# Kernel optimization log

Hardware: AMD Instinct MI355X
Metric: run time of the kernel (lower is better)

The kernel has to match this reference:

```python
import jax, jax.numpy as jnp
import numpy as np

LOSS_WEIGHT = 1.0

# Zero-padded shifts implementing PyTorch cross-correlation stencils.
# _shift_w(x, +1)[..., j] = x[..., j+1] (zero outside), etc.

def _shift_w(x, s):
    if s == 1:
        return jnp.pad(x[..., 1:], ((0, 0), (0, 0), (0, 1)))
    return jnp.pad(x[..., :-1], ((0, 0), (0, 0), (1, 0)))


def _shift_h(x, s):
    if s == 1:
        return jnp.pad(x[..., 1:, :], ((0, 0), (0, 1), (0, 0)))
    return jnp.pad(x[..., :-1, :], ((0, 0), (1, 0), (0, 0)))


def _curvature_loss(prob):
    # prob: [B, H, W]. Fused stencil chain equivalent to the 7 tiny conv2d calls.
    lap = (_shift_h(prob, 1) + _shift_h(prob, -1)
           + _shift_w(prob, 1) + _shift_w(prob, -1) - 4.0 * prob)
    gx = _shift_w(lap, 1) - _shift_w(lap, -1)          # dx = [-1, 0, 1]
    gy = _shift_h(lap, 1) - _shift_h(lap, -1)          # dy = [-1, 0, 1]^T
    hxx = 2.0 * gx - _shift_w(gx, 1) - _shift_w(gx, -1)  # dxx = [-1, 2, -1]
    hyy = 2.0 * gy - _shift_h(gy, 1) - _shift_h(gy, -1)  # dyy = [-1, 2, -1]^T
    hxy = _shift_w(gx, 1) - _shift_w(gx, -1)
    numerator = hxx * (1.0 + gy) ** 2 - 2.0 * hxy * gx * gy + hyy * (1.0 + gx) ** 2
    denominator = 2.0 * (1.0 + gx ** 2 + gy ** 2) ** 1.5
    curvature = numerator / denominator
    neg_curv = jnp.maximum(-curvature, 0.0)
    s = jnp.sum(neg_curv, axis=(1, 2))                              # [B]
    c = jnp.sum(neg_curv != 0, axis=(1, 2)).astype(prob.dtype)      # [B]
    # per-sample masked mean, skipped when no negative curvature
    per_sample = jnp.where(c > 0, s / jnp.maximum(c, 1.0), 0.0)
    return jnp.sum(per_sample)


def setup_inputs() -> dict:
    key = jax.random.key(0)
    k1, k2 = jax.random.split(key)
    pred = jax.random.normal(k1, (8, 4, 1024, 1024), dtype=jnp.float32)
    target = jax.random.randint(k2, (8, 1024, 1024), 0, 4, dtype=jnp.int64)
    return {"pred": pred, "target": target}


def reference(pred, target):
    # softmax=True path; num_classes == 4 branch of the original forward
    p = jax.nn.softmax(pred, axis=1)
    prob_1 = p[:, 1]
    prob_2 = p[:, 1] + p[:, 2]
    prob_3 = p[:, 3]
    loss = (_curvature_loss(prob_1) + _curvature_loss(prob_2)
            + _curvature_loss(prob_3))
    return loss * LOSS_WEIGHT
```

## Files before the change

kernel.cpp:

```cpp
#include <hip/hip_runtime.h>


namespace {
constexpr int H = 1024, W = 1024, B = 8;
constexpr int VALID = 120;
constexpr int NSTRIPS = 9;
constexpr int RCHUNK = 8;
constexpr int NCHUNKS = H / RCHUNK;
constexpr int WPB = 4;
constexpr int NTHREADS = 64 * WPB;
constexpr size_t HW = (size_t)H * W;
}

__device__ __forceinline__ float dpp_left(float x) {
    return __builtin_bit_cast(float,
        __builtin_amdgcn_update_dpp(0, __builtin_bit_cast(int, x),
                                    0x138 , 0xf, 0xf, false));
}
__device__ __forceinline__ float dpp_right(float x) {
    return __builtin_bit_cast(float,
        __builtin_amdgcn_update_dpp(0, __builtin_bit_cast(int, x),
                                    0x130 , 0xf, 0xf, false));
}

__global__ void zero_ws_kernel(unsigned int* ws) {
    if (threadIdx.x < 48) ws[threadIdx.x] = 0u;
}

__device__ __forceinline__ float2 ld2(const float* p) {
    return *(const float2*)p;
}

template <bool RE>
__device__ __forceinline__ void load_row4(const float* __restrict__ basep, int row,
                                          float2 o[4]) {
    const int rc = RE ? min(max(row, 0), H - 1) : row;
    const float* p = basep + (size_t)rc * W;
    o[0] = ld2(p);
    o[1] = ld2(p + HW);
    o[2] = ld2(p + 2 * HW);
    o[3] = ld2(p + 3 * HW);
}

template <bool CE>
__device__ __forceinline__ void softmax_pair(const float2 x[4], bool ok0, bool ok1,
                                             float2 p[3]) {
    const float e0x = __expf(x[0].x), e1x = __expf(x[1].x);
    const float e2x = __expf(x[2].x), e3x = __expf(x[3].x);
    const float e0y = __expf(x[0].y), e1y = __expf(x[1].y);
    const float e2y = __expf(x[2].y), e3y = __expf(x[3].y);
    const float ix = __builtin_amdgcn_rcpf(e0x + e1x + e2x + e3x);
    const float iy = __builtin_amdgcn_rcpf(e0y + e1y + e2y + e3y);
    if (CE) {
        p[0].x = ok0 ? e1x * ix : 0.f;
        p[0].y = ok1 ? e1y * iy : 0.f;
        p[1].x = ok0 ? (e1x + e2x) * ix : 0.f;
        p[1].y = ok1 ? (e1y + e2y) * iy : 0.f;
        p[2].x = ok0 ? e3x * ix : 0.f;
        p[2].y = ok1 ? e3y * iy : 0.f;
    } else {
        p[0].x = e1x * ix;            p[0].y = e1y * iy;
        p[1].x = (e1x + e2x) * ix;    p[1].y = (e1y + e2y) * iy;
        p[2].x = e3x * ix;            p[2].y = e3y * iy;
    }
}

template <bool CE, bool RE>
__device__ __forceinline__ void sweep(const float* __restrict__ pred,
                                      int b, int strip, int chunk, int lane,
                                      float sacc[3], unsigned int cacc[3]) {
    const int r0 = chunk * RCHUNK;
    const int li0 = 2 * lane;
    const int col0 = strip * VALID - 4 + li0;
    const int col1 = col0 + 1;
    const int colC = CE ? min(max(col0, 0), W - 2) : col0;
    const float* basep = pred + (size_t)b * 4 * HW + colC;

    const bool cOK0 = !CE || ((unsigned)col0 < (unsigned)W);
    const bool cOK1 = !CE || ((unsigned)col1 < (unsigned)W);
    const bool aOK0 = (li0 >= 4) && (li0 <= 123) && cOK0;
    const bool aOK1 = (li0 + 1 >= 4) && (li0 + 1 <= 123) && cOK1;
    const float gxpM0 = (!CE || (col0 + 1 < W)) ? 1.f : 0.f;
    const float gxpM1 = (!CE || (col1 + 1 < W)) ? 1.f : 0.f;
    const float gxmM0 = (!CE || (col0 >= 1)) ? 1.f : 0.f;
    const float gxmM1 = (!CE || (col1 >= 1)) ? 1.f : 0.f;

    float2 P[3][3];
    float2 L[6][3];
    float2 Rr[2][4];

    {
        float2 t[4];
        load_row4<RE>(basep, r0 - 3, t);
        const bool ok = !RE || ((unsigned)(r0 - 3) < (unsigned)H);
        softmax_pair<CE || RE>(t, ok && cOK0, ok && cOK1, P[1]);
        load_row4<RE>(basep, r0 - 2, t);
        const bool ok2 = !RE || ((unsigned)(r0 - 2) < (unsigned)H);
        softmax_pair<CE || RE>(t, ok2 && cOK0, ok2 && cOK1, P[2]);
    }
    load_row4<RE>(basep, r0 - 1, Rr[0]);
    load_row4<RE>(basep, r0, Rr[1]);

    auto acc1 = [&](int f, float gx, float gy, float gxp, float gxm,
                    float gyp, float gym, bool aOK) {
        const float hxx = 2.f * gx - gxp - gxm;
        const float hxy = gxp - gxm;
        const float hyy = 2.f * gy - gyp - gym;
        const float oy = 1.f + gy, ox = 1.f + gx;
        const float numer = hxx * oy * oy - 2.f * hxy * gx * gy + hyy * ox * ox;
        const float xx = 1.f + gx * gx + gy * gy;
        const float rs = __builtin_amdgcn_rsqf(xx);
        const float curv = numer * (0.5f * rs * rs * rs);
        const float negc = aOK ? fmaxf(-curv, 0.f) : 0.f;
        sacc[f] += negc;
        cacc[f] += (negc != 0.f) ? 1u : 0u;
    };

    for (int m = 0; m < 2; ++m) {
#pragma unroll
        for (int u = 0; u < 6; ++u) {
            const int y = r0 - 4 + m * 6 + u;
            const bool pok = !RE || ((unsigned)(y + 3) < (unsigned)H);
            softmax_pair<CE || RE>(Rr[u % 2], pok && cOK0, pok && cOK1, P[u % 3]);
            load_row4<RE>(basep, y + 5, Rr[u % 2]);
            const bool lok = !RE || ((unsigned)(y + 2) < (unsigned)H);
#pragma unroll
            for (int f = 0; f < 3; ++f) {
                const float2 top = P[(u + 1) % 3][f];
                const float2 mid = P[(u + 2) % 3][f];
                const float2 bot = P[u % 3][f];
                const float lft = dpp_left(mid.y);
                const float rgt = dpp_right(mid.x);
                const float lx = top.x + bot.x + lft + mid.y - 4.f * mid.x;
                const float ly = top.y + bot.y + mid.x + rgt - 4.f * mid.y;
                if (CE || RE) {
                    L[u][f].x = (lok && cOK0) ? lx : 0.f;
                    L[u][f].y = (lok && cOK1) ? ly : 0.f;
                } else {
                    L[u][f].x = lx;
                    L[u][f].y = ly;
                }
            }
            if (m > 0 || u >= 4) {
                const float gypM = (!RE || (y + 1 < H)) ? 1.f : 0.f;
                const float gymM = (!RE || (y >= 1)) ? 1.f : 0.f;
#pragma unroll
                for (int f = 0; f < 3; ++f) {
                    const float2 lm2 = L[(u + 2) % 6][f];
                    const float2 lm1 = L[(u + 3) % 6][f];
                    const float2 lc  = L[(u + 4) % 6][f];
                    const float2 lp1 = L[(u + 5) % 6][f];
                    const float2 lp2 = L[u % 6][f];
                    const float A  = dpp_left(lc.y);
                    const float Bm = dpp_left(lc.x);
                    const float Bp = dpp_right(lc.x);
                    const float Cc = dpp_right(lc.y);
                    {
                        const float c = lc.x;
                        const float gx = lc.y - A;
                        const float gy = lp1.x - lm1.x;
                        const float gxp = (Bp - c) * gxpM0;
                        const float gxm = (c - Bm) * gxmM0;
                        const float gyp = (lp2.x - c) * gypM;
                        const float gym = (c - lm2.x) * gymM;
                        acc1(f, gx, gy, gxp, gxm, gyp, gym, aOK0);
                    }
                    {
                        const float c = lc.y;
                        const float gx = Bp - lc.x;
                        const float gy = lp1.y - lm1.y;
                        const float gxp = (Cc - c) * gxpM1;
                        const float gxm = (c - A) * gxmM1;
                        const float gyp = (lp2.y - c) * gypM;
                        const float gym = (c - lm2.y) * gymM;
                        acc1(f, gx, gy, gxp, gxm, gyp, gym, aOK1);
                    }
                }
            }
        }
    }
}

__global__ __launch_bounds__(NTHREADS)
void curvature_sweep(const float* __restrict__ pred,
                     float* __restrict__ s_ws,
                     unsigned int* __restrict__ c_ws) {
    __shared__ float redS[3][WPB];
    __shared__ unsigned int redC[3][WPB];

    const int strip = blockIdx.x;
    const int b = blockIdx.z;
    const int tid = threadIdx.x;
    const int wv = tid >> 6, lane = tid & 63;
    const int chunk = blockIdx.y * WPB + wv;

    const bool ce = (strip == 0) || (strip == NSTRIPS - 1);
    const bool re = (chunk == 0) || (chunk == NCHUNKS - 1);

    float sacc[3] = {0.f, 0.f, 0.f};
    unsigned int cacc[3] = {0u, 0u, 0u};
    if (!ce && !re)      sweep<false, false>(pred, b, strip, chunk, lane, sacc, cacc);
    else if (ce && !re)  sweep<true, false>(pred, b, strip, chunk, lane, sacc, cacc);
    else if (!ce && re)  sweep<false, true>(pred, b, strip, chunk, lane, sacc, cacc);
    else                 sweep<true, true>(pred, b, strip, chunk, lane, sacc, cacc);

#pragma unroll
    for (int f = 0; f < 3; ++f) {
        float v = sacc[f];
        unsigned int c = cacc[f];
        for (int off = 32; off > 0; off >>= 1) {
            v += __shfl_xor(v, off, 64);
            c += __shfl_xor(c, off, 64);
        }
        if (lane == 0) { redS[f][wv] = v; redC[f][wv] = c; }
    }
    __syncthreads();
    if (tid < 3) {
        float v = 0.f;
        unsigned int c = 0;
        for (int w2 = 0; w2 < WPB; ++w2) { v += redS[tid][w2]; c += redC[tid][w2]; }
        atomicAdd(&s_ws[b * 3 + tid], v);
        atomicAdd(&c_ws[b * 3 + tid], c);
    }
}

__global__ void finalize_kernel(const float* __restrict__ s_ws,
                                const unsigned int* __restrict__ c_ws,
                                float* __restrict__ out) {
    const int lane = threadIdx.x;
    float v = 0.f;
    if (lane < 24) {
        const float s = s_ws[lane];
        const unsigned int c = c_ws[lane];
        v = (c > 0) ? s / (float)c : 0.f;
    }
    for (int off = 32; off > 0; off >>= 1) v += __shfl_down(v, off, 64);
    if (lane == 0) out[0] = v;
}

extern "C" void kernel_launch(void* const* d_in, const int* in_sizes, int n_in,
                              void* d_out, int out_size, void* d_ws, size_t ws_size,
                              hipStream_t stream) {
    const float* pred = (const float*)d_in[0];
    float* s_ws = (float*)d_ws;
    unsigned int* c_ws = (unsigned int*)((char*)d_ws + 24 * sizeof(float));
    float* out = (float*)d_out;

    hipLaunchKernelGGL(zero_ws_kernel, dim3(1), dim3(64), 0, stream,
                       (unsigned int*)d_ws);
    dim3 grid(NSTRIPS, NCHUNKS / WPB, B);
    hipLaunchKernelGGL(curvature_sweep, grid, dim3(NTHREADS), 0, stream,
                       pred, s_ws, c_ws);
    hipLaunchKernelGGL(finalize_kernel, dim3(1), dim3(64), 0, stream,
                       s_ws, c_ws, out);
}
```

Measured before the change: 68.43 us.

## Double row chunk height and vectorize stencil math with packed float2 ops

Each wave now sweeps 16 rows instead of 8, with the ring buffers resized to 5 slots and an unrolled 10-step inner loop. This cuts the share of halo rows that are recomputed (softmax and Laplacian) per output row. The per-pixel curvature math is rewritten on 2-wide ext_vector floats so the compiler can emit packed FP32 instructions. A min-blocks-per-SM hint is added to launch bounds. In exchange there are half as many work items, which lowers available parallelism, and register pressure may rise.

```diff
diff --git a/kernel.cpp b/kernel.cpp
--- a/kernel.cpp
+++ b/kernel.cpp
@@ -5,13 +5,19 @@
 constexpr int H = 1024, W = 1024, B = 8;
 constexpr int VALID = 120;
 constexpr int NSTRIPS = 9;
-constexpr int RCHUNK = 8;
+constexpr int RCHUNK = 16;
 constexpr int NCHUNKS = H / RCHUNK;
 constexpr int WPB = 4;
 constexpr int NTHREADS = 64 * WPB;
 constexpr size_t HW = (size_t)H * W;
 }
 
+using v2f = __attribute__((ext_vector_type(2))) float;
+
+__device__ __forceinline__ v2f mk2(float a, float b) {
+    v2f r; r.x = a; r.y = b; return r;
+}
+
 __device__ __forceinline__ float dpp_left(float x) {
     return __builtin_bit_cast(float,
         __builtin_amdgcn_update_dpp(0, __builtin_bit_cast(int, x),
@@ -27,48 +33,42 @@
     if (threadIdx.x < 48) ws[threadIdx.x] = 0u;
 }
 
-__device__ __forceinline__ float2 ld2(const float* p) {
-    return *(const float2*)p;
-}
-
 template <bool RE>
 __device__ __forceinline__ void load_row4(const float* __restrict__ basep, int row,
-                                          float2 o[4]) {
+                                          v2f o[4]) {
     const int rc = RE ? min(max(row, 0), H - 1) : row;
     const float* p = basep + (size_t)rc * W;
-    o[0] = ld2(p);
-    o[1] = ld2(p + HW);
-    o[2] = ld2(p + 2 * HW);
-    o[3] = ld2(p + 3 * HW);
-}
-
-template <bool CE>
-__device__ __forceinline__ void softmax_pair(const float2 x[4], bool ok0, bool ok1,
-                                             float2 p[3]) {
+    o[0] = *(const v2f*)p;
+    o[1] = *(const v2f*)(p + HW);
+    o[2] = *(const v2f*)(p + 2 * HW);
+    o[3] = *(const v2f*)(p + 3 * HW);
+}
+
+template <bool EDGE>
+__device__ __forceinline__ void softmax_pair(const v2f x[4], bool ok0, bool ok1,
+                                             v2f p[3]) {
     const float e0x = __expf(x[0].x), e1x = __expf(x[1].x);
     const float e2x = __expf(x[2].x), e3x = __expf(x[3].x);
     const float e0y = __expf(x[0].y), e1y = __expf(x[1].y);
     const float e2y = __expf(x[2].y), e3y = __expf(x[3].y);
     const float ix = __builtin_amdgcn_rcpf(e0x + e1x + e2x + e3x);
     const float iy = __builtin_amdgcn_rcpf(e0y + e1y + e2y + e3y);
-    if (CE) {
-        p[0].x = ok0 ? e1x * ix : 0.f;
-        p[0].y = ok1 ? e1y * iy : 0.f;
-        p[1].x = ok0 ? (e1x + e2x) * ix : 0.f;
-        p[1].y = ok1 ? (e1y + e2y) * iy : 0.f;
-        p[2].x = ok0 ? e3x * ix : 0.f;
-        p[2].y = ok1 ? e3y * iy : 0.f;
+    if (EDGE) {
+        p[0] = mk2(ok0 ? e1x * ix : 0.f,          ok1 ? e1y * iy : 0.f);
+        p[1] = mk2(ok0 ? (e1x + e2x) * ix : 0.f,  ok1 ? (e1y + e2y) * iy : 0.f);
+        p[2] = mk2(ok0 ? e3x * ix : 0.f,          ok1 ? e3y * iy : 0.f);
     } else {
-        p[0].x = e1x * ix;            p[0].y = e1y * iy;
-        p[1].x = (e1x + e2x) * ix;    p[1].y = (e1y + e2y) * iy;
-        p[2].x = e3x * ix;            p[2].y = e3y * iy;
+        p[0] = mk2(e1x * ix,          e1y * iy);
+        p[1] = mk2((e1x + e2x) * ix,  (e1y + e2y) * iy);
+        p[2] = mk2(e3x * ix,          e3y * iy);
     }
 }
 
 template <bool CE, bool RE>
 __device__ __forceinline__ void sweep(const float* __restrict__ pred,
                                       int b, int strip, int chunk, int lane,
-                                      float sacc[3], unsigned int cacc[3]) {
+                                      v2f sacc[3], unsigned int cacc0[3],
+                                      unsigned int cacc1[3]) {
     const int r0 = chunk * RCHUNK;
     const int li0 = 2 * lane;
     const int col0 = strip * VALID - 4 + li0;
@@ -80,65 +80,50 @@
     const bool cOK1 = !CE || ((unsigned)col1 < (unsigned)W);
     const bool aOK0 = (li0 >= 4) && (li0 <= 123) && cOK0;
     const bool aOK1 = (li0 + 1 >= 4) && (li0 + 1 <= 123) && cOK1;
-    const float gxpM0 = (!CE || (col0 + 1 < W)) ? 1.f : 0.f;
-    const float gxpM1 = (!CE || (col1 + 1 < W)) ? 1.f : 0.f;
-    const float gxmM0 = (!CE || (col0 >= 1)) ? 1.f : 0.f;
-    const float gxmM1 = (!CE || (col1 >= 1)) ? 1.f : 0.f;
-
-    float2 P[3][3];
-    float2 L[6][3];
-    float2 Rr[2][4];
+    const v2f aM = mk2(aOK0 ? 1.f : 0.f, aOK1 ? 1.f : 0.f);
+    const v2f gxpM = mk2((!CE || (col0 + 1 < W)) ? 1.f : 0.f,
+                         (!CE || (col1 + 1 < W)) ? 1.f : 0.f);
+    const v2f gxmM = mk2((!CE || (col0 >= 1)) ? 1.f : 0.f,
+                         (!CE || (col1 >= 1)) ? 1.f : 0.f);
+
+    v2f P[5][3];
+    v2f L[5][3];
+    v2f Rr[2][4];
 
     {
-        float2 t[4];
+        v2f t[4];
         load_row4<RE>(basep, r0 - 3, t);
         const bool ok = !RE || ((unsigned)(r0 - 3) < (unsigned)H);
-        softmax_pair<CE || RE>(t, ok && cOK0, ok && cOK1, P[1]);
+        softmax_pair<CE || RE>(t, ok && cOK0, ok && cOK1, P[3]);
         load_row4<RE>(basep, r0 - 2, t);
         const bool ok2 = !RE || ((unsigned)(r0 - 2) < (unsigned)H);
-        softmax_pair<CE || RE>(t, ok2 && cOK0, ok2 && cOK1, P[2]);
+        softmax_pair<CE || RE>(t, ok2 && cOK0, ok2 && cOK1, P[4]);
     }
     load_row4<RE>(basep, r0 - 1, Rr[0]);
     load_row4<RE>(basep, r0, Rr[1]);
 
-    auto acc1 = [&](int f, float gx, float gy, float gxp, float gxm,
-                    float gyp, float gym, bool aOK) {
-        const float hxx = 2.f * gx - gxp - gxm;
-        const float hxy = gxp - gxm;
-        const float hyy = 2.f * gy - gyp - gym;
-        const float oy = 1.f + gy, ox = 1.f + gx;
-        const float numer = hxx * oy * oy - 2.f * hxy * gx * gy + hyy * ox * ox;
-        const float xx = 1.f + gx * gx + gy * gy;
-        const float rs = __builtin_amdgcn_rsqf(xx);
-        const float curv = numer * (0.5f * rs * rs * rs);
-        const float negc = aOK ? fmaxf(-curv, 0.f) : 0.f;
-        sacc[f] += negc;
-        cacc[f] += (negc != 0.f) ? 1u : 0u;
-    };
-
     for (int m = 0; m < 2; ++m) {
 #pragma unroll
-        for (int u = 0; u < 6; ++u) {
-            const int y = r0 - 4 + m * 6 + u;
+        for (int u = 0; u < 10; ++u) {
+            const int y = r0 - 4 + m * 10 + u;
             const bool pok = !RE || ((unsigned)(y + 3) < (unsigned)H);
-            softmax_pair<CE || RE>(Rr[u % 2], pok && cOK0, pok && cOK1, P[u % 3]);
+            softmax_pair<CE || RE>(Rr[u % 2], pok && cOK0, pok && cOK1, P[u % 5]);
             load_row4<RE>(basep, y + 5, Rr[u % 2]);
             const bool lok = !RE || ((unsigned)(y + 2) < (unsigned)H);
 #pragma unroll
             for (int f = 0; f < 3; ++f) {
-                const float2 top = P[(u + 1) % 3][f];
-                const float2 mid = P[(u + 2) % 3][f];
-                const float2 bot = P[u % 3][f];
+                const v2f top = P[(u + 3) % 5][f];
+                const v2f mid = P[(u + 4) % 5][f];
+                const v2f bot = P[u % 5][f];
                 const float lft = dpp_left(mid.y);
                 const float rgt = dpp_right(mid.x);
-                const float lx = top.x + bot.x + lft + mid.y - 4.f * mid.x;
-                const float ly = top.y + bot.y + mid.x + rgt - 4.f * mid.y;
+                const v2f horiz = mk2(lft, mid.x) + mk2(mid.y, rgt);
+                const v2f l = top + bot + horiz - 4.f * mid;
                 if (CE || RE) {
-                    L[u][f].x = (lok && cOK0) ? lx : 0.f;
-                    L[u][f].y = (lok && cOK1) ? ly : 0.f;
+                    L[u % 5][f] = mk2((lok && cOK0) ? l.x : 0.f,
+                                      (lok && cOK1) ? l.y : 0.f);
                 } else {
-                    L[u][f].x = lx;
-                    L[u][f].y = ly;
+                    L[u % 5][f] = l;
                 }
             }
             if (m > 0 || u >= 4) {
@@ -146,42 +131,46 @@
                 const float gymM = (!RE || (y >= 1)) ? 1.f : 0.f;
 #pragma unroll
                 for (int f = 0; f < 3; ++f) {
-                    const float2 lm2 = L[(u + 2) % 6][f];
-                    const float2 lm1 = L[(u + 3) % 6][f];
-                    const float2 lc  = L[(u + 4) % 6][f];
-                    const float2 lp1 = L[(u + 5) % 6][f];
-                    const float2 lp2 = L[u % 6][f];
+                    const v2f lm2 = L[(u + 1) % 5][f];
+                    const v2f lm1 = L[(u + 2) % 5][f];
+                    const v2f lc  = L[(u + 3) % 5][f];
+                    const v2f lp1 = L[(u + 4) % 5][f];
+                    const v2f lp2 = L[u % 5][f];
                     const float A  = dpp_left(lc.y);
                     const float Bm = dpp_left(lc.x);
                     const float Bp = dpp_right(lc.x);
                     const float Cc = dpp_right(lc.y);
-                    {
-                        const float c = lc.x;
-                        const float gx = lc.y - A;
-                        const float gy = lp1.x - lm1.x;
-                        const float gxp = (Bp - c) * gxpM0;
-                        const float gxm = (c - Bm) * gxmM0;
-                        const float gyp = (lp2.x - c) * gypM;
-                        const float gym = (c - lm2.x) * gymM;
-                        acc1(f, gx, gy, gxp, gxm, gyp, gym, aOK0);
-                    }
-                    {
-                        const float c = lc.y;
-                        const float gx = Bp - lc.x;
-                        const float gy = lp1.y - lm1.y;
-                        const float gxp = (Cc - c) * gxpM1;
-                        const float gxm = (c - A) * gxmM1;
-                        const float gyp = (lp2.y - c) * gypM;
-                        const float gym = (c - lm2.y) * gymM;
-                        acc1(f, gx, gy, gxp, gxm, gyp, gym, aOK1);
-                    }
+                    const v2f c   = lc;
+                    const v2f gx  = mk2(lc.y, Bp) - mk2(A, lc.x);
+                    const v2f gy  = lp1 - lm1;
+                    const v2f gxp = (mk2(Bp, Cc) - c) * gxpM;
+                    const v2f gxm = (c - mk2(Bm, A)) * gxmM;
+                    const v2f gyp = (lp2 - c) * gypM;
+                    const v2f gym = (c - lm2) * gymM;
+                    const v2f hxx = 2.f * gx - gxp - gxm;
+                    const v2f hxy = gxp - gxm;
+                    const v2f hyy = 2.f * gy - gyp - gym;
+                    const v2f ox = 1.f + gx, oy = 1.f + gy;
+                    const v2f numer = hxx * oy * oy - 2.f * hxy * (gx * gy)
+                                    + hyy * ox * ox;
+                    const v2f xx = 1.f + gx * gx + gy * gy;
+                    const float rs0 = __builtin_amdgcn_rsqf(xx.x);
+                    const float rs1 = __builtin_amdgcn_rsqf(xx.y);
+                    const v2f invden = mk2(0.5f * rs0 * rs0 * rs0,
+                                           0.5f * rs1 * rs1 * rs1);
+                    const v2f curv = numer * invden;
+                    const v2f negc = mk2(fmaxf(-curv.x, 0.f),
+                                         fmaxf(-curv.y, 0.f)) * aM;
+                    sacc[f] += negc;
+                    cacc0[f] += (negc.x != 0.f) ? 1u : 0u;
+                    cacc1[f] += (negc.y != 0.f) ? 1u : 0u;
                 }
             }
         }
     }
 }
 
-__global__ __launch_bounds__(NTHREADS)
+__global__ __launch_bounds__(NTHREADS, 4)
 void curvature_sweep(const float* __restrict__ pred,
                      float* __restrict__ s_ws,
                      unsigned int* __restrict__ c_ws) {
@@ -197,17 +186,22 @@
     const bool ce = (strip == 0) || (strip == NSTRIPS - 1);
     const bool re = (chunk == 0) || (chunk == NCHUNKS - 1);
 
-    float sacc[3] = {0.f, 0.f, 0.f};
-    unsigned int cacc[3] = {0u, 0u, 0u};
-    if (!ce && !re)      sweep<false, false>(pred, b, strip, chunk, lane, sacc, cacc);
-    else if (ce && !re)  sweep<true, false>(pred, b, strip, chunk, lane, sacc, cacc);
-    else if (!ce && re)  sweep<false, true>(pred, b, strip, chunk, lane, sacc, cacc);
-    else                 sweep<true, true>(pred, b, strip, chunk, lane, sacc, cacc);
+    v2f sacc[3] = {mk2(0.f, 0.f), mk2(0.f, 0.f), mk2(0.f, 0.f)};
+    unsigned int cacc0[3] = {0u, 0u, 0u};
+    unsigned int cacc1[3] = {0u, 0u, 0u};
+    if (!ce && !re)
+        sweep<false, false>(pred, b, strip, chunk, lane, sacc, cacc0, cacc1);
+    else if (ce && !re)
+        sweep<true, false>(pred, b, strip, chunk, lane, sacc, cacc0, cacc1);
+    else if (!ce && re)
+        sweep<false, true>(pred, b, strip, chunk, lane, sacc, cacc0, cacc1);
+    else
+        sweep<true, true>(pred, b, strip, chunk, lane, sacc, cacc0, cacc1);
 
 #pragma unroll
     for (int f = 0; f < 3; ++f) {
-        float v = sacc[f];
-        unsigned int c = cacc[f];
+        float v = sacc[f].x + sacc[f].y;
+        unsigned int c = cacc0[f] + cacc1[f];
         for (int off = 32; off > 0; off >>= 1) {
             v += __shfl_xor(v, off, 64);
             c += __shfl_xor(c, off, 64);
```

After: 56.42 us. 17.5% less time.
